# Performance work log

Hardware: AMD Instinct MI355X
Metric: run time of the kernel (lower is better)

The kernel has to match this reference:

```python
import jax, jax.numpy as jnp
import numpy as np

T, B, D, H = 2048, 32, 512, 512


def setup_inputs() -> dict:
    key = jax.random.key(0)
    k0, k1, k2, k3 = jax.random.split(key, 4)
    inp = jax.random.normal(k0, (T, B, D), dtype=jnp.float32) * 0.1
    paddings = (jax.random.uniform(k1, (T, B, 1)) > 0.9).astype(jnp.float32)
    W_x = jax.random.normal(k2, (D, 4 * H), dtype=jnp.float32) / np.sqrt(D)
    W_h = jax.random.normal(k3, (H, 4 * H), dtype=jnp.float32) / np.sqrt(H)
    b = jnp.zeros((4 * H,), dtype=jnp.float32)
    return {"input": inp, "paddings": paddings, "W_x": W_x, "W_h": W_h, "b": b}


def reference(input, paddings, W_x, W_h, b):
    """Masked LSTM recurrence over time.

    input:    [T, B, D]
    paddings: [T, B, 1] (1.0 = padded -> carry previous state)
    returns (outputs [T, B, H], (m [B, H], c [B, H]))
    """
    batch = input.shape[1]
    m0 = jnp.zeros((batch, H), dtype=input.dtype)
    c0 = jnp.zeros((batch, H), dtype=input.dtype)

    # Precompute input projections for all timesteps in one big GEMM.
    x_proj = jnp.einsum('tbd,dk->tbk', input, W_x) + b  # [T, B, 4H]

    def step(carry, xt_pt):
        m, c = carry
        xp, p = xt_pt                      # xp: [B, 4H], p: [B, 1]
        gates = xp + m @ W_h               # [B, 4H]
        i, f, g, o = jnp.split(gates, 4, axis=-1)
        c_new = jax.nn.sigmoid(f) * c + jax.nn.sigmoid(i) * jnp.tanh(g)
        m_new = jax.nn.sigmoid(o) * jnp.tanh(c_new)
        m2 = m_new * (1.0 - p) + m * p
        c2 = c_new * (1.0 - p) + c * p
        return (m2, c2), m2

    (m_f, c_f), outputs = jax.lax.scan(step, (m0, c0), (x_proj, paddings))
    return outputs, (m_f, c_f)
```

## Files before the change

kernel.cpp:

```cpp
#include <hip/hip_runtime.h>


typedef __bf16  bf16x8 __attribute__((ext_vector_type(8)));
typedef float   f32x4  __attribute__((ext_vector_type(4)));

__device__ __forceinline__ unsigned short f2bf(float f) {
  unsigned u = __builtin_bit_cast(unsigned, f);
  u += 0x7fffu + ((u >> 16) & 1u);
  return (unsigned short)(u >> 16);
}
__device__ __forceinline__ float bf2f(unsigned short h) {
  unsigned u = ((unsigned)h) << 16;
  return __builtin_bit_cast(float, u);
}
__device__ __forceinline__ float fast_sigmoid(float x) {
  return __builtin_amdgcn_rcpf(1.0f + __expf(-x));
}
__device__ __forceinline__ float fast_tanh(float x) {
  return 2.0f * __builtin_amdgcn_rcpf(1.0f + __expf(-2.0f * x)) - 1.0f;
}

__global__ __launch_bounds__(256) void transpose_cvt(
    const float* __restrict__ Wx, const float* __restrict__ Wh,
    unsigned short* __restrict__ WxT, unsigned short* __restrict__ WhT) {
  const float* src = blockIdx.z ? Wh : Wx;
  unsigned short* dst = blockIdx.z ? WhT : WxT;
  __shared__ float tile[32][33];
  const int n0 = blockIdx.x * 32, k0 = blockIdx.y * 32;
  const int t = threadIdx.x;
  {
    const int kk = t >> 3, nn = (t & 7) * 4;
    float4 v = *(const float4*)(src + (size_t)(k0 + kk) * 2048 + n0 + nn);
    tile[kk][nn + 0] = v.x; tile[kk][nn + 1] = v.y;
    tile[kk][nn + 2] = v.z; tile[kk][nn + 3] = v.w;
  }
  __syncthreads();
  {
    const int n = t >> 3, k4 = (t & 7) * 4;
    ushort4 o;
    o.x = f2bf(tile[k4 + 0][n]); o.y = f2bf(tile[k4 + 1][n]);
    o.z = f2bf(tile[k4 + 2][n]); o.w = f2bf(tile[k4 + 3][n]);
    *(ushort4*)(dst + (size_t)(n0 + n) * 512 + k0 + k4) = o;
  }
}

__global__ __launch_bounds__(256) void gemm_xproj(
    const float* __restrict__ A, const unsigned short* __restrict__ BT,
    const float* __restrict__ bias, unsigned short* __restrict__ C) {
  __shared__ unsigned short As[128 * 32];
  __shared__ unsigned short Bs[128 * 32];
  const int m0 = blockIdx.x * 128, n0 = blockIdx.y * 128;
  const int tid = threadIdx.x, w = tid >> 6, lane = tid & 63;
  const int q = lane >> 4, r = lane & 15;
  const int wm = (w >> 1) * 64, wn = (w & 1) * 64;
  const int srow = tid >> 1, shalf = tid & 1;

  f32x4 acc[4][4] = {};

  for (int kt = 0; kt < 16; ++kt) {
    const int k0 = kt * 32;
    {
      const float* ap = A + (size_t)(m0 + srow) * 512 + k0 + shalf * 16;
#pragma unroll
      for (int c = 0; c < 4; ++c) {
        float4 v = *(const float4*)(ap + c * 4);
        ushort4 h;
        h.x = f2bf(v.x); h.y = f2bf(v.y); h.z = f2bf(v.z); h.w = f2bf(v.w);
        *(ushort4*)&As[srow * 32 + shalf * 16 + c * 4] = h;
      }
    }
    {
      const unsigned short* bp = BT + (size_t)(n0 + srow) * 512 + k0 + shalf * 16;
#pragma unroll
      for (int c2 = 0; c2 < 2; ++c2)
        *(uint4*)&Bs[srow * 32 + shalf * 16 + c2 * 8] = *(const uint4*)(bp + c2 * 8);
    }
    __syncthreads();
    bf16x8 af[4], bfr[4];
#pragma unroll
    for (int i = 0; i < 4; ++i)
      af[i] = *(const bf16x8*)&As[(wm + i * 16 + r) * 32 + q * 8];
#pragma unroll
    for (int j = 0; j < 4; ++j)
      bfr[j] = *(const bf16x8*)&Bs[(wn + j * 16 + r) * 32 + q * 8];
#pragma unroll
    for (int i = 0; i < 4; ++i)
#pragma unroll
      for (int j = 0; j < 4; ++j)
        acc[i][j] = __builtin_amdgcn_mfma_f32_16x16x32_bf16(af[i], bfr[j], acc[i][j], 0, 0, 0);
    __syncthreads();
  }
#pragma unroll
  for (int j = 0; j < 4; ++j) {
    const int col = n0 + wn + j * 16 + r;
    const float bv = bias[col];
#pragma unroll
    for (int i = 0; i < 4; ++i) {
#pragma unroll
      for (int e = 0; e < 4; ++e) {
        const int row = m0 + wm + i * 16 + q * 4 + e;
        C[(size_t)row * 2048 + col] = f2bf(acc[i][j][e] + bv);
      }
    }
  }
}

__global__ __launch_bounds__(256, 1) void lstm_rec(
    const unsigned short* __restrict__ xp,
    const float* __restrict__ pads,
    const unsigned short* __restrict__ WhT,
    float* __restrict__ out,
    unsigned short* __restrict__ mb0, unsigned short* __restrict__ mb1,
    unsigned int* __restrict__ slots) {
  const int g = blockIdx.x, tid = threadIdx.x;
  const int w = tid >> 6, lane = tid & 63, q = lane >> 4, r = lane & 15;

  __shared__ unsigned mA[8192];
  __shared__ float gsm[64 * 33];

  const int n_loc = w * 16 + r;
  const int h_loc = n_loc >> 2, typ = n_loc & 3;
  const int n_glob = typ * 512 + g * 16 + h_loc;
  bf16x8 bfrag[16];
#pragma unroll
  for (int kt = 0; kt < 16; ++kt)
    bfrag[kt] = *(const bf16x8*)(WhT + (size_t)n_glob * 512 + kt * 32 + q * 8);

  const int row = lane >> 1;
  const int hglob = g * 16 + w * 4 + (lane & 1) * 2;
  const size_t mwoff = (size_t)((hglob >> 5) * 2 + (row >> 4)) * 1024 +
                       (size_t)(((hglob >> 3) & 3) * 16 + (row & 15)) * 16 +
                       (size_t)(hglob & 7) * 2;
  float cst0 = 0.f, cst1 = 0.f, mst0 = 0.f, mst1 = 0.f;

  float pf_p = pads[row];
  unsigned pf_x[4];
#pragma unroll
  for (int ty = 0; ty < 4; ++ty)
    pf_x[ty] = *(const unsigned*)(xp + (size_t)row * 2048 + ty * 512 + hglob);

  for (int t = 0; t < 2048; ++t) {
    const unsigned* mr = (const unsigned*)((t & 1) ? mb1 : mb0);
    unsigned* mw = (unsigned*)((t & 1) ? mb0 : mb1);

    unsigned mt[32];
#pragma unroll
    for (int i = 0; i < 32; ++i)
      mt[i] = __hip_atomic_load(mr + i * 256 + tid, __ATOMIC_RELAXED,
                                __HIP_MEMORY_SCOPE_AGENT);
#pragma unroll
    for (int i = 0; i < 32; ++i)
      mA[i * 256 + tid] = mt[i];
    __syncthreads();

    f32x4 acc0 = {}, acc1 = {};
#pragma unroll
    for (int kt = 0; kt < 16; ++kt) {
      bf16x8 a0 = *(const bf16x8*)((const char*)mA + (size_t)(kt * 2 + 0) * 1024 + lane * 16);
      bf16x8 a1 = *(const bf16x8*)((const char*)mA + (size_t)(kt * 2 + 1) * 1024 + lane * 16);
      acc0 = __builtin_amdgcn_mfma_f32_16x16x32_bf16(a0, bfrag[kt], acc0, 0, 0, 0);
      acc1 = __builtin_amdgcn_mfma_f32_16x16x32_bf16(a1, bfrag[kt], acc1, 0, 0, 0);
    }
#pragma unroll
    for (int e = 0; e < 4; ++e) {
      gsm[n_loc * 33 + q * 4 + e]      = acc0[e];
      gsm[n_loc * 33 + 16 + q * 4 + e] = acc1[e];
    }
    const float* gcol = gsm + (size_t)(w * 16 + (lane & 1) * 8) * 33 + row;
    float gt[8];
#pragma unroll
    for (int j = 0; j < 8; ++j) gt[j] = gcol[j * 33];

    {
      const float p = pf_p;
      const float xi0 = bf2f((unsigned short)(pf_x[0] & 0xffff));
      const float xi1 = bf2f((unsigned short)(pf_x[0] >> 16));
      const float xf0 = bf2f((unsigned short)(pf_x[1] & 0xffff));
      const float xf1 = bf2f((unsigned short)(pf_x[1] >> 16));
      const float xg0 = bf2f((unsigned short)(pf_x[2] & 0xffff));
      const float xg1 = bf2f((unsigned short)(pf_x[2] >> 16));
      const float xo0 = bf2f((unsigned short)(pf_x[3] & 0xffff));
      const float xo1 = bf2f((unsigned short)(pf_x[3] >> 16));

      const float si0 = fast_sigmoid(gt[0] + xi0), sf0 = fast_sigmoid(gt[1] + xf0);
      const float tg0 = fast_tanh(gt[2] + xg0),    so0 = fast_sigmoid(gt[3] + xo0);
      const float si1 = fast_sigmoid(gt[4] + xi1), sf1 = fast_sigmoid(gt[5] + xf1);
      const float tg1 = fast_tanh(gt[6] + xg1),    so1 = fast_sigmoid(gt[7] + xo1);

      const float cn0 = sf0 * cst0 + si0 * tg0;
      const float cn1 = sf1 * cst1 + si1 * tg1;
      const float mn0 = so0 * fast_tanh(cn0);
      const float mn1 = so1 * fast_tanh(cn1);
      const float m20 = mn0 + p * (mst0 - mn0), c20 = cn0 + p * (cst0 - cn0);
      const float m21 = mn1 + p * (mst1 - mn1), c21 = cn1 + p * (cst1 - cn1);
      cst0 = c20; mst0 = m20; cst1 = c21; mst1 = m21;

      *(float2*)(out + (size_t)t * 16384 + (size_t)row * 512 + hglob) =
          make_float2(m20, m21);
      const unsigned pack = (unsigned)f2bf(m20) | ((unsigned)f2bf(m21) << 16);
      __hip_atomic_store((unsigned*)((char*)mw + mwoff), pack,
                         __ATOMIC_RELAXED, __HIP_MEMORY_SCOPE_AGENT);
    }

    {
      const int tn = (t + 1) & 2047;
      pf_p = pads[tn * 32 + row];
#pragma unroll
      for (int ty = 0; ty < 4; ++ty)
        pf_x[ty] = *(const unsigned*)(xp + (size_t)(tn * 32 + row) * 2048 + ty * 512 + hglob);
    }

    __threadfence_block();
    __syncthreads();
    if (tid == 0)
      __hip_atomic_store(slots + g * 16, (unsigned)(t + 1),
                         __ATOMIC_RELAXED, __HIP_MEMORY_SCOPE_AGENT);
    if (tid < 64) {
      const unsigned tgt = (unsigned)(t + 1);
      for (;;) {
        unsigned v = (tid < 32)
            ? __hip_atomic_load(slots + tid * 16, __ATOMIC_RELAXED,
                                __HIP_MEMORY_SCOPE_AGENT)
            : tgt;
        if (__ballot(v < tgt) == 0ull) break;
        __builtin_amdgcn_s_sleep(1);
      }
    }
    __syncthreads();
  }

  {
    float* mo = out + 33554432 + (size_t)row * 512 + hglob;
    *(float2*)mo = make_float2(mst0, mst1);
    *(float2*)(mo + 16384) = make_float2(cst0, cst1);
  }
}

extern "C" void kernel_launch(void* const* d_in, const int* in_sizes, int n_in,
                              void* d_out, int out_size, void* d_ws, size_t ws_size,
                              hipStream_t stream) {
  (void)in_sizes; (void)n_in; (void)out_size; (void)ws_size;
  const float* input = (const float*)d_in[0];
  const float* pads  = (const float*)d_in[1];
  const float* Wx    = (const float*)d_in[2];
  const float* Wh    = (const float*)d_in[3];
  const float* bias  = (const float*)d_in[4];
  float* out = (float*)d_out;

  char* ws = (char*)d_ws;
  unsigned short* xp  = (unsigned short*)(ws);
  unsigned short* WxT = (unsigned short*)(ws + 268435456);
  unsigned short* WhT = (unsigned short*)(ws + 270532608);
  unsigned short* mb0 = (unsigned short*)(ws + 272629760);
  unsigned short* mb1 = (unsigned short*)(ws + 272662528);
  unsigned int* slots = (unsigned int*)(ws + 272695296);

  hipMemsetAsync(ws + 272629760, 0, 32768 * 2 + 2048, stream);

  transpose_cvt<<<dim3(64, 16, 2), 256, 0, stream>>>(Wx, Wh, WxT, WhT);
  gemm_xproj<<<dim3(512, 16), 256, 0, stream>>>(input, WxT, bias, xp);
  lstm_rec<<<32, 256, 0, stream>>>(xp, pads, WhT, out, mb0, mb1, slots);
}
```

Measured before the change: 7.087 ms.

## Split LSTM recurrence into two independent batch groups with per-wave flag sync

The recurrent kernel now runs 64 blocks as two independent groups of 16 batch rows each, so each group exchanges a smaller hidden-state buffer and synchronizes only within itself. The block-wide __syncthreads barrier and single per-block slot are replaced by per-wave flags that each wave publishes after its own state store, and every wave spins on all 128 flags of its group. The MFMA loop uses four accumulators to break the dependency chain, and the gate transpose through shared memory is done per wave. The intent is to shorten the per-timestep critical path and cut synchronization latency, at the cost of more polling traffic and twice as many blocks each doing a full-size W_h fragment load.

```diff
diff --git a/kernel.cpp b/kernel.cpp
--- a/kernel.cpp
+++ b/kernel.cpp
@@ -110,129 +110,118 @@
     const float* __restrict__ pads,
     const unsigned short* __restrict__ WhT,
     float* __restrict__ out,
-    unsigned short* __restrict__ mb0, unsigned short* __restrict__ mb1,
-    unsigned int* __restrict__ slots) {
-  const int g = blockIdx.x, tid = threadIdx.x;
-  const int w = tid >> 6, lane = tid & 63, q = lane >> 4, r = lane & 15;
-
-  __shared__ unsigned mA[8192];
-  __shared__ float gsm[64 * 33];
-
-  const int n_loc = w * 16 + r;
-  const int h_loc = n_loc >> 2, typ = n_loc & 3;
-  const int n_glob = typ * 512 + g * 16 + h_loc;
+    unsigned short* __restrict__ mbuf,
+    unsigned int* __restrict__ flags) {
+  const int bid = blockIdx.x, grp = bid >> 5, g = bid & 31;
+  const int tid = threadIdx.x, w = tid >> 6, lane = tid & 63;
+  const int q = lane >> 4, r = lane & 15;
+
+  __shared__ unsigned long long mAq[2048];
+  __shared__ float gsm[4 * 16 * 17];
+
+  const int typ_b = r & 3, hl_b = r >> 2;
+  const int n_glob = typ_b * 512 + g * 16 + w * 4 + hl_b;
   bf16x8 bfrag[16];
 #pragma unroll
   for (int kt = 0; kt < 16; ++kt)
     bfrag[kt] = *(const bf16x8*)(WhT + (size_t)n_glob * 512 + kt * 32 + q * 8);
 
-  const int row = lane >> 1;
-  const int hglob = g * 16 + w * 4 + (lane & 1) * 2;
-  const size_t mwoff = (size_t)((hglob >> 5) * 2 + (row >> 4)) * 1024 +
-                       (size_t)(((hglob >> 3) & 3) * 16 + (row & 15)) * 16 +
-                       (size_t)(hglob & 7) * 2;
-  float cst0 = 0.f, cst1 = 0.f, mst0 = 0.f, mst1 = 0.f;
-
-  float pf_p = pads[row];
-  unsigned pf_x[4];
+  const int erow = lane >> 2, ehl = lane & 3;
+  const int h = g * 16 + w * 4 + ehl;
+  const int brow = grp * 16 + erow;
+  const size_t mwoff = (size_t)(h >> 5) * 1024 +
+                       (size_t)(((h >> 3) & 3) * 16 + erow) * 16 +
+                       (size_t)(h & 7) * 2;
+  float cst = 0.f, mst = 0.f;
+
+  const unsigned wid = (unsigned)(g * 4 + w);
+  unsigned int* const gflags = flags + grp * 128;
+  unsigned short* const gbuf = mbuf + (size_t)grp * 16384;
+
+  float pf_p = pads[brow];
+  unsigned short pf_x[4];
 #pragma unroll
   for (int ty = 0; ty < 4; ++ty)
-    pf_x[ty] = *(const unsigned*)(xp + (size_t)row * 2048 + ty * 512 + hglob);
+    pf_x[ty] = xp[(size_t)brow * 2048 + ty * 512 + h];
 
   for (int t = 0; t < 2048; ++t) {
-    const unsigned* mr = (const unsigned*)((t & 1) ? mb1 : mb0);
-    unsigned* mw = (unsigned*)((t & 1) ? mb0 : mb1);
-
-    unsigned mt[32];
-#pragma unroll
-    for (int i = 0; i < 32; ++i)
-      mt[i] = __hip_atomic_load(mr + i * 256 + tid, __ATOMIC_RELAXED,
+    const unsigned long long* mr =
+        (const unsigned long long*)(gbuf + ((t & 1) ? 8192 : 0));
+    unsigned long long mt[8];
+#pragma unroll
+    for (int c = 0; c < 8; ++c)
+      mt[c] = __hip_atomic_load(mr + c * 256 + tid, __ATOMIC_RELAXED,
                                 __HIP_MEMORY_SCOPE_AGENT);
 #pragma unroll
-    for (int i = 0; i < 32; ++i)
-      mA[i * 256 + tid] = mt[i];
+    for (int c = 0; c < 8; ++c)
+      mAq[c * 256 + tid] = mt[c];
     __syncthreads();
 
-    f32x4 acc0 = {}, acc1 = {};
+    f32x4 ac[4] = {};
 #pragma unroll
     for (int kt = 0; kt < 16; ++kt) {
-      bf16x8 a0 = *(const bf16x8*)((const char*)mA + (size_t)(kt * 2 + 0) * 1024 + lane * 16);
-      bf16x8 a1 = *(const bf16x8*)((const char*)mA + (size_t)(kt * 2 + 1) * 1024 + lane * 16);
-      acc0 = __builtin_amdgcn_mfma_f32_16x16x32_bf16(a0, bfrag[kt], acc0, 0, 0, 0);
-      acc1 = __builtin_amdgcn_mfma_f32_16x16x32_bf16(a1, bfrag[kt], acc1, 0, 0, 0);
-    }
-#pragma unroll
-    for (int e = 0; e < 4; ++e) {
-      gsm[n_loc * 33 + q * 4 + e]      = acc0[e];
-      gsm[n_loc * 33 + 16 + q * 4 + e] = acc1[e];
-    }
-    const float* gcol = gsm + (size_t)(w * 16 + (lane & 1) * 8) * 33 + row;
-    float gt[8];
-#pragma unroll
-    for (int j = 0; j < 8; ++j) gt[j] = gcol[j * 33];
-
-    {
-      const float p = pf_p;
-      const float xi0 = bf2f((unsigned short)(pf_x[0] & 0xffff));
-      const float xi1 = bf2f((unsigned short)(pf_x[0] >> 16));
-      const float xf0 = bf2f((unsigned short)(pf_x[1] & 0xffff));
-      const float xf1 = bf2f((unsigned short)(pf_x[1] >> 16));
-      const float xg0 = bf2f((unsigned short)(pf_x[2] & 0xffff));
-      const float xg1 = bf2f((unsigned short)(pf_x[2] >> 16));
-      const float xo0 = bf2f((unsigned short)(pf_x[3] & 0xffff));
-      const float xo1 = bf2f((unsigned short)(pf_x[3] >> 16));
-
-      const float si0 = fast_sigmoid(gt[0] + xi0), sf0 = fast_sigmoid(gt[1] + xf0);
-      const float tg0 = fast_tanh(gt[2] + xg0),    so0 = fast_sigmoid(gt[3] + xo0);
-      const float si1 = fast_sigmoid(gt[4] + xi1), sf1 = fast_sigmoid(gt[5] + xf1);
-      const float tg1 = fast_tanh(gt[6] + xg1),    so1 = fast_sigmoid(gt[7] + xo1);
-
-      const float cn0 = sf0 * cst0 + si0 * tg0;
-      const float cn1 = sf1 * cst1 + si1 * tg1;
-      const float mn0 = so0 * fast_tanh(cn0);
-      const float mn1 = so1 * fast_tanh(cn1);
-      const float m20 = mn0 + p * (mst0 - mn0), c20 = cn0 + p * (cst0 - cn0);
-      const float m21 = mn1 + p * (mst1 - mn1), c21 = cn1 + p * (cst1 - cn1);
-      cst0 = c20; mst0 = m20; cst1 = c21; mst1 = m21;
-
-      *(float2*)(out + (size_t)t * 16384 + (size_t)row * 512 + hglob) =
-          make_float2(m20, m21);
-      const unsigned pack = (unsigned)f2bf(m20) | ((unsigned)f2bf(m21) << 16);
-      __hip_atomic_store((unsigned*)((char*)mw + mwoff), pack,
-                         __ATOMIC_RELAXED, __HIP_MEMORY_SCOPE_AGENT);
-    }
-
-    {
-      const int tn = (t + 1) & 2047;
-      pf_p = pads[tn * 32 + row];
+      bf16x8 a = *(const bf16x8*)((const char*)mAq + kt * 1024 + lane * 16);
+      ac[kt & 3] = __builtin_amdgcn_mfma_f32_16x16x32_bf16(a, bfrag[kt], ac[kt & 3], 0, 0, 0);
+    }
+    const f32x4 acc = (ac[0] + ac[1]) + (ac[2] + ac[3]);
+
+    float* gw = gsm + w * 272;
+#pragma unroll
+    for (int e = 0; e < 4; ++e)
+      gw[r * 17 + q * 4 + e] = acc[e];
+    const float gt0 = gw[(ehl * 4 + 0) * 17 + erow];
+    const float gt1 = gw[(ehl * 4 + 1) * 17 + erow];
+    const float gt2 = gw[(ehl * 4 + 2) * 17 + erow];
+    const float gt3 = gw[(ehl * 4 + 3) * 17 + erow];
+
+    const float p  = pf_p;
+    const float xi = bf2f(pf_x[0]), xf = bf2f(pf_x[1]);
+    const float xg = bf2f(pf_x[2]), xo = bf2f(pf_x[3]);
+    const float si = fast_sigmoid(gt0 + xi), sf = fast_sigmoid(gt1 + xf);
+    const float tg = fast_tanh(gt2 + xg),    so = fast_sigmoid(gt3 + xo);
+    const float cn = sf * cst + si * tg;
+    const float mn = so * fast_tanh(cn);
+    const float m2 = mn + p * (mst - mn);
+    const float c2 = cn + p * (cst - cn);
+    mst = m2; cst = c2;
+
+    if (t < 2047) {
+      unsigned short* mw = gbuf + (((t + 1) & 1) ? 8192 : 0);
+      const unsigned mu = (unsigned)f2bf(m2);
+      const unsigned hi = (unsigned)__shfl_down((int)mu, 1);
+      if ((lane & 1) == 0)
+        __hip_atomic_store((unsigned*)((char*)mw + mwoff), mu | (hi << 16),
+                           __ATOMIC_RELAXED, __HIP_MEMORY_SCOPE_AGENT);
+      asm volatile("s_waitcnt vmcnt(0)" ::: "memory");
+      if (lane == 0)
+        __hip_atomic_store(gflags + wid, (unsigned)(t + 1),
+                           __ATOMIC_RELAXED, __HIP_MEMORY_SCOPE_AGENT);
+    }
+
+    out[(size_t)t * 16384 + (size_t)brow * 512 + h] = m2;
+
+    if (t < 2047) {
+      pf_p = pads[(t + 1) * 32 + brow];
 #pragma unroll
       for (int ty = 0; ty < 4; ++ty)
-        pf_x[ty] = *(const unsigned*)(xp + (size_t)(tn * 32 + row) * 2048 + ty * 512 + hglob);
-    }
-
-    __threadfence_block();
-    __syncthreads();
-    if (tid == 0)
-      __hip_atomic_store(slots + g * 16, (unsigned)(t + 1),
-                         __ATOMIC_RELAXED, __HIP_MEMORY_SCOPE_AGENT);
-    if (tid < 64) {
+        pf_x[ty] = xp[(size_t)((t + 1) * 32 + brow) * 2048 + ty * 512 + h];
+
       const unsigned tgt = (unsigned)(t + 1);
       for (;;) {
-        unsigned v = (tid < 32)
-            ? __hip_atomic_load(slots + tid * 16, __ATOMIC_RELAXED,
-                                __HIP_MEMORY_SCOPE_AGENT)
-            : tgt;
-        if (__ballot(v < tgt) == 0ull) break;
+        const unsigned v0 = __hip_atomic_load(gflags + lane, __ATOMIC_RELAXED,
+                                              __HIP_MEMORY_SCOPE_AGENT);
+        const unsigned v1 = __hip_atomic_load(gflags + 64 + lane, __ATOMIC_RELAXED,
+                                              __HIP_MEMORY_SCOPE_AGENT);
+        if (__ballot((v0 < tgt) || (v1 < tgt)) == 0ull) break;
         __builtin_amdgcn_s_sleep(1);
       }
     }
-    __syncthreads();
   }
 
   {
-    float* mo = out + 33554432 + (size_t)row * 512 + hglob;
-    *(float2*)mo = make_float2(mst0, mst1);
-    *(float2*)(mo + 16384) = make_float2(cst0, cst1);
+    float* mo = out + 33554432 + (size_t)brow * 512 + h;
+    mo[0]     = mst;
+    mo[16384] = cst;
   }
 }
 
@@ -251,13 +240,12 @@
   unsigned short* xp  = (unsigned short*)(ws);
   unsigned short* WxT = (unsigned short*)(ws + 268435456);
   unsigned short* WhT = (unsigned short*)(ws + 270532608);
-  unsigned short* mb0 = (unsigned short*)(ws + 272629760);
-  unsigned short* mb1 = (unsigned short*)(ws + 272662528);
-  unsigned int* slots = (unsigned int*)(ws + 272695296);
-
-  hipMemsetAsync(ws + 272629760, 0, 32768 * 2 + 2048, stream);
+  unsigned short* mb  = (unsigned short*)(ws + 272629760);
+  unsigned int* flags = (unsigned int*)(ws + 272695296);
+
+  hipMemsetAsync(ws + 272629760, 0, 65536 + 2048, stream);
 
   transpose_cvt<<<dim3(64, 16, 2), 256, 0, stream>>>(Wx, Wh, WxT, WhT);
   gemm_xproj<<<dim3(512, 16), 256, 0, stream>>>(input, WxT, bias, xp);
-  lstm_rec<<<32, 256, 0, stream>>>(xp, pads, WhT, out, mb0, mb1, slots);
-}
+  lstm_rec<<<64, 256, 0, stream>>>(xp, pads, WhT, out, mb, flags);
+}
```

New measurement: 8.711 ms. 1.23x slower.

## Replace slot-counter grid barrier with per-element tagged hidden-state publication

Applied to the files above, without the earlier changes.

Each published hidden-state word now carries the timestep as a 32-bit tag in a 64-bit slot, so consumers spin directly on the data until every tag matches instead of going through a separate counter barrier plus two block syncs. The next step's state is speculatively loaded right after the store, the LDS staging buffer is double-buffered so a single barrier per step suffices, and the MFMA chain is split into two independent accumulators. This removes a global round-trip and barrier latency on the serial critical path, but doubles the traffic per state element and makes correctness depend on ordering of relaxed 64-bit atomics.

```diff
diff --git a/kernel.cpp b/kernel.cpp
--- a/kernel.cpp
+++ b/kernel.cpp
@@ -110,12 +110,11 @@
     const float* __restrict__ pads,
     const unsigned short* __restrict__ WhT,
     float* __restrict__ out,
-    unsigned short* __restrict__ mb0, unsigned short* __restrict__ mb1,
-    unsigned int* __restrict__ slots) {
+    unsigned long long* __restrict__ tb) {
   const int g = blockIdx.x, tid = threadIdx.x;
   const int w = tid >> 6, lane = tid & 63, q = lane >> 4, r = lane & 15;
 
-  __shared__ unsigned mA[8192];
+  __shared__ unsigned mAv[2 * 8192];
   __shared__ float gsm[64 * 33];
 
   const int n_loc = w * 16 + r;
@@ -128,9 +127,11 @@
 
   const int row = lane >> 1;
   const int hglob = g * 16 + w * 4 + (lane & 1) * 2;
-  const size_t mwoff = (size_t)((hglob >> 5) * 2 + (row >> 4)) * 1024 +
-                       (size_t)(((hglob >> 3) & 3) * 16 + (row & 15)) * 16 +
-                       (size_t)(hglob & 7) * 2;
+  const unsigned mwoff = (unsigned)((hglob >> 5) * 2 + (row >> 4)) * 1024u +
+                         (unsigned)(((hglob >> 3) & 3) * 16 + (row & 15)) * 16u +
+                         (unsigned)(hglob & 7) * 2u;
+  unsigned long long* const pub0 =
+      (unsigned long long*)((char*)tb + (size_t)mwoff * 2);
   float cst0 = 0.f, cst1 = 0.f, mst0 = 0.f, mst1 = 0.f;
 
   float pf_p = pads[row];
@@ -139,28 +140,54 @@
   for (int ty = 0; ty < 4; ++ty)
     pf_x[ty] = *(const unsigned*)(xp + (size_t)row * 2048 + ty * 512 + hglob);
 
+  unsigned long long mt[32];
+#pragma unroll
+  for (int c = 0; c < 32; ++c)
+    mt[c] = __hip_atomic_load(tb + c * 256 + tid, __ATOMIC_RELAXED,
+                              __HIP_MEMORY_SCOPE_AGENT);
+
   for (int t = 0; t < 2048; ++t) {
-    const unsigned* mr = (const unsigned*)((t & 1) ? mb1 : mb0);
-    unsigned* mw = (unsigned*)((t & 1) ? mb0 : mb1);
-
-    unsigned mt[32];
-#pragma unroll
-    for (int i = 0; i < 32; ++i)
-      mt[i] = __hip_atomic_load(mr + i * 256 + tid, __ATOMIC_RELAXED,
-                                __HIP_MEMORY_SCOPE_AGENT);
-#pragma unroll
-    for (int i = 0; i < 32; ++i)
-      mA[i * 256 + tid] = mt[i];
-    __syncthreads();
-
-    f32x4 acc0 = {}, acc1 = {};
-#pragma unroll
-    for (int kt = 0; kt < 16; ++kt) {
-      bf16x8 a0 = *(const bf16x8*)((const char*)mA + (size_t)(kt * 2 + 0) * 1024 + lane * 16);
-      bf16x8 a1 = *(const bf16x8*)((const char*)mA + (size_t)(kt * 2 + 1) * 1024 + lane * 16);
-      acc0 = __builtin_amdgcn_mfma_f32_16x16x32_bf16(a0, bfrag[kt], acc0, 0, 0, 0);
-      acc1 = __builtin_amdgcn_mfma_f32_16x16x32_bf16(a1, bfrag[kt], acc1, 0, 0, 0);
-    }
+    const unsigned tagv = (unsigned)t;
+    const unsigned long long* trd = tb + (size_t)(t & 1) * 8192;
+
+    for (;;) {
+      bool bad = false;
+#pragma unroll
+      for (int c = 0; c < 32; ++c)
+        bad |= ((unsigned)(mt[c] >> 32) != tagv);
+      if (__ballot(bad) == 0ull) break;
+      if (bad) {
+#pragma unroll
+        for (int c = 0; c < 32; ++c)
+          mt[c] = __hip_atomic_load(trd + c * 256 + tid, __ATOMIC_RELAXED,
+                                    __HIP_MEMORY_SCOPE_AGENT);
+      }
+    }
+
+    unsigned* dsd = &mAv[(t & 1) * 8192];
+#pragma unroll
+    for (int c = 0; c < 32; ++c)
+      dsd[c * 256 + tid] = (unsigned)mt[c];
+    asm volatile("s_waitcnt lgkmcnt(0)" ::: "memory");
+    __builtin_amdgcn_sched_barrier(0);
+    __builtin_amdgcn_s_barrier();
+    __builtin_amdgcn_sched_barrier(0);
+
+    const char* mbase = (const char*)&mAv[(t & 1) * 8192];
+    f32x4 a00 = {}, a01 = {}, a10 = {}, a11 = {};
+#pragma unroll
+    for (int kt = 0; kt < 16; kt += 2) {
+      bf16x8 a0 = *(const bf16x8*)(mbase + (size_t)(kt * 2 + 0) * 1024 + lane * 16);
+      bf16x8 a1 = *(const bf16x8*)(mbase + (size_t)(kt * 2 + 1) * 1024 + lane * 16);
+      a00 = __builtin_amdgcn_mfma_f32_16x16x32_bf16(a0, bfrag[kt], a00, 0, 0, 0);
+      a10 = __builtin_amdgcn_mfma_f32_16x16x32_bf16(a1, bfrag[kt], a10, 0, 0, 0);
+      bf16x8 a2 = *(const bf16x8*)(mbase + (size_t)(kt * 2 + 2) * 1024 + lane * 16);
+      bf16x8 a3 = *(const bf16x8*)(mbase + (size_t)(kt * 2 + 3) * 1024 + lane * 16);
+      a01 = __builtin_amdgcn_mfma_f32_16x16x32_bf16(a2, bfrag[kt + 1], a01, 0, 0, 0);
+      a11 = __builtin_amdgcn_mfma_f32_16x16x32_bf16(a3, bfrag[kt + 1], a11, 0, 0, 0);
+    }
+    const f32x4 acc0 = a00 + a01, acc1 = a10 + a11;
+
 #pragma unroll
     for (int e = 0; e < 4; ++e) {
       gsm[n_loc * 33 + q * 4 + e]      = acc0[e];
@@ -171,62 +198,51 @@
 #pragma unroll
     for (int j = 0; j < 8; ++j) gt[j] = gcol[j * 33];
 
-    {
-      const float p = pf_p;
-      const float xi0 = bf2f((unsigned short)(pf_x[0] & 0xffff));
-      const float xi1 = bf2f((unsigned short)(pf_x[0] >> 16));
-      const float xf0 = bf2f((unsigned short)(pf_x[1] & 0xffff));
-      const float xf1 = bf2f((unsigned short)(pf_x[1] >> 16));
-      const float xg0 = bf2f((unsigned short)(pf_x[2] & 0xffff));
-      const float xg1 = bf2f((unsigned short)(pf_x[2] >> 16));
-      const float xo0 = bf2f((unsigned short)(pf_x[3] & 0xffff));
-      const float xo1 = bf2f((unsigned short)(pf_x[3] >> 16));
-
-      const float si0 = fast_sigmoid(gt[0] + xi0), sf0 = fast_sigmoid(gt[1] + xf0);
-      const float tg0 = fast_tanh(gt[2] + xg0),    so0 = fast_sigmoid(gt[3] + xo0);
-      const float si1 = fast_sigmoid(gt[4] + xi1), sf1 = fast_sigmoid(gt[5] + xf1);
-      const float tg1 = fast_tanh(gt[6] + xg1),    so1 = fast_sigmoid(gt[7] + xo1);
-
-      const float cn0 = sf0 * cst0 + si0 * tg0;
-      const float cn1 = sf1 * cst1 + si1 * tg1;
-      const float mn0 = so0 * fast_tanh(cn0);
-      const float mn1 = so1 * fast_tanh(cn1);
-      const float m20 = mn0 + p * (mst0 - mn0), c20 = cn0 + p * (cst0 - cn0);
-      const float m21 = mn1 + p * (mst1 - mn1), c21 = cn1 + p * (cst1 - cn1);
-      cst0 = c20; mst0 = m20; cst1 = c21; mst1 = m21;
-
-      *(float2*)(out + (size_t)t * 16384 + (size_t)row * 512 + hglob) =
-          make_float2(m20, m21);
-      const unsigned pack = (unsigned)f2bf(m20) | ((unsigned)f2bf(m21) << 16);
-      __hip_atomic_store((unsigned*)((char*)mw + mwoff), pack,
+    const float p = pf_p;
+    const float xi0 = bf2f((unsigned short)(pf_x[0] & 0xffff));
+    const float xi1 = bf2f((unsigned short)(pf_x[0] >> 16));
+    const float xf0 = bf2f((unsigned short)(pf_x[1] & 0xffff));
+    const float xf1 = bf2f((unsigned short)(pf_x[1] >> 16));
+    const float xg0 = bf2f((unsigned short)(pf_x[2] & 0xffff));
+    const float xg1 = bf2f((unsigned short)(pf_x[2] >> 16));
+    const float xo0 = bf2f((unsigned short)(pf_x[3] & 0xffff));
+    const float xo1 = bf2f((unsigned short)(pf_x[3] >> 16));
+
+    const float si0 = fast_sigmoid(gt[0] + xi0), sf0 = fast_sigmoid(gt[1] + xf0);
+    const float tg0 = fast_tanh(gt[2] + xg0),    so0 = fast_sigmoid(gt[3] + xo0);
+    const float si1 = fast_sigmoid(gt[4] + xi1), sf1 = fast_sigmoid(gt[5] + xf1);
+    const float tg1 = fast_tanh(gt[6] + xg1),    so1 = fast_sigmoid(gt[7] + xo1);
+
+    const float cn0 = sf0 * cst0 + si0 * tg0;
+    const float cn1 = sf1 * cst1 + si1 * tg1;
+    const float mn0 = so0 * fast_tanh(cn0);
+    const float mn1 = so1 * fast_tanh(cn1);
+    const float m20 = mn0 + p * (mst0 - mn0), c20 = cn0 + p * (cst0 - cn0);
+    const float m21 = mn1 + p * (mst1 - mn1), c21 = cn1 + p * (cst1 - cn1);
+    cst0 = c20; mst0 = m20; cst1 = c21; mst1 = m21;
+
+    if (t < 2047) {
+      const unsigned pd = (unsigned)f2bf(m20) | ((unsigned)f2bf(m21) << 16);
+      const unsigned long long val =
+          (unsigned long long)pd | ((unsigned long long)(unsigned)(t + 1) << 32);
+      __hip_atomic_store(pub0 + (size_t)((t + 1) & 1) * 8192, val,
                          __ATOMIC_RELAXED, __HIP_MEMORY_SCOPE_AGENT);
-    }
-
-    {
-      const int tn = (t + 1) & 2047;
-      pf_p = pads[tn * 32 + row];
+      const unsigned long long* nrd = tb + (size_t)((t + 1) & 1) * 8192;
+#pragma unroll
+      for (int c = 0; c < 32; ++c)
+        mt[c] = __hip_atomic_load(nrd + c * 256 + tid, __ATOMIC_RELAXED,
+                                  __HIP_MEMORY_SCOPE_AGENT);
+    }
+
+    *(float2*)(out + (size_t)t * 16384 + (size_t)row * 512 + hglob) =
+        make_float2(m20, m21);
+
+    if (t < 2047) {
+      pf_p = pads[(t + 1) * 32 + row];
 #pragma unroll
       for (int ty = 0; ty < 4; ++ty)
-        pf_x[ty] = *(const unsigned*)(xp + (size_t)(tn * 32 + row) * 2048 + ty * 512 + hglob);
-    }
-
-    __threadfence_block();
-    __syncthreads();
-    if (tid == 0)
-      __hip_atomic_store(slots + g * 16, (unsigned)(t + 1),
-                         __ATOMIC_RELAXED, __HIP_MEMORY_SCOPE_AGENT);
-    if (tid < 64) {
-      const unsigned tgt = (unsigned)(t + 1);
-      for (;;) {
-        unsigned v = (tid < 32)
-            ? __hip_atomic_load(slots + tid * 16, __ATOMIC_RELAXED,
-                                __HIP_MEMORY_SCOPE_AGENT)
-            : tgt;
-        if (__ballot(v < tgt) == 0ull) break;
-        __builtin_amdgcn_s_sleep(1);
-      }
-    }
-    __syncthreads();
+        pf_x[ty] = *(const unsigned*)(xp + (size_t)((t + 1) * 32 + row) * 2048 + ty * 512 + hglob);
+    }
   }
 
   {
@@ -251,13 +267,11 @@
   unsigned short* xp  = (unsigned short*)(ws);
   unsigned short* WxT = (unsigned short*)(ws + 268435456);
   unsigned short* WhT = (unsigned short*)(ws + 270532608);
-  unsigned short* mb0 = (unsigned short*)(ws + 272629760);
-  unsigned short* mb1 = (unsigned short*)(ws + 272662528);
-  unsigned int* slots = (unsigned int*)(ws + 272695296);
-
-  hipMemsetAsync(ws + 272629760, 0, 32768 * 2 + 2048, stream);
+  unsigned long long* tb = (unsigned long long*)(ws + 272629760);
+
+  hipMemsetAsync(ws + 272629760, 0, 131072, stream);
 
   transpose_cvt<<<dim3(64, 16, 2), 256, 0, stream>>>(Wx, Wh, WxT, WhT);
   gemm_xproj<<<dim3(512, 16), 256, 0, stream>>>(input, WxT, bias, xp);
-  lstm_rec<<<32, 256, 0, stream>>>(xp, pads, WhT, out, mb0, mb1, slots);
-}
+  lstm_rec<<<32, 256, 0, stream>>>(xp, pads, WhT, out, tb);
+}
```

New measurement: 9.004 ms. +27.0%, slower.
